# Kernel tuning notes

Hardware: AMD Instinct MI355X
Metric: run time of the kernel (lower is better)

Reference implementation:

```python
import jax, jax.numpy as jnp
import numpy as np

EMBED_DIM = 1024


def setup_inputs() -> dict:
    key = jax.random.key(0)
    ks = jax.random.split(key, 9)
    d = EMBED_DIM
    s = 1.0 / np.sqrt(d)
    x = jax.random.normal(ks[0], (4, 2048, d), dtype=jnp.float32)
    # nn.Linear weights are [out, in]; we store them transposed for x @ W
    Wq = jax.random.uniform(ks[1], (d, d), jnp.float32, -s, s)
    bq = jax.random.uniform(ks[2], (d,), jnp.float32, -s, s)
    Wk = jax.random.uniform(ks[3], (d, d), jnp.float32, -s, s)
    bk = jax.random.uniform(ks[4], (d,), jnp.float32, -s, s)
    Wv = jax.random.uniform(ks[5], (d, d), jnp.float32, -s, s)
    bv = jax.random.uniform(ks[6], (d,), jnp.float32, -s, s)
    Wo = jax.random.uniform(ks[7], (d, d), jnp.float32, -s, s)
    bo = jax.random.uniform(ks[8], (d,), jnp.float32, -s, s)
    return {"x": x, "Wq": Wq, "bq": bq, "Wk": Wk, "bk": bk,
            "Wv": Wv, "bv": bv, "Wo": Wo, "bo": bo}


def reference(x, Wq, bq, Wk, bk, Wv, bv, Wo, bo):
    b, seq_len, d = x.shape
    scaling = 1.0 / jnp.sqrt(jnp.float32(d))
    q = x @ Wq + bq  # [b, s, d]
    k = x @ Wk + bk
    v = x @ Wv + bv
    scores = jnp.einsum('bqd,bkd->bqk', q, k) * scaling  # [b, s, s]
    causal = jnp.tril(jnp.ones((seq_len, seq_len), dtype=bool))
    scores = jnp.where(causal, scores, -jnp.inf)
    attn = jax.nn.softmax(scores, axis=-1)
    out = jnp.einsum('bqk,bkd->bqd', attn, v)
    return out @ Wo + bo
```

## Files before the change

### kernel.cpp

```cpp
#include <hip/hip_runtime.h>
#include <stdint.h>

typedef __bf16 bf16_t;
typedef __bf16 bf16x8 __attribute__((ext_vector_type(8)));
typedef __bf16 bf16x4 __attribute__((ext_vector_type(4)));
typedef float  f32x4  __attribute__((ext_vector_type(4)));

#define DEV __device__ __forceinline__

constexpr int S = 2048, D = 1024, BATCH = 4, MF = BATCH * S;

DEV void gload16(const void* g, void* l) {
  __builtin_amdgcn_global_load_lds(
      (const __attribute__((address_space(1))) void*)g,
      (__attribute__((address_space(3))) void*)(uint32_t)(uintptr_t)l,
      16, 0, 0);
}

template<int EP>
__global__ __launch_bounds__(256, 4) void gemm_core(
    const bf16_t* __restrict__ A, const bf16_t* __restrict__ B,
    void* __restrict__ C0, void* __restrict__ C1, void* __restrict__ C2,
    const float* __restrict__ aux, float* __restrict__ part,
    int M, int N, int K, long sA, long sB)
{
  int tm = blockIdx.x, tn = blockIdx.y;
  const int bz = blockIdx.z;
  if (EP == 2) {
    const int t = blockIdx.x;
    tm = (int)((sqrtf(8.0f * t + 1.0f) - 1.0f) * 0.5f);
    while ((tm + 1) * (tm + 2) / 2 <= t) ++tm;
    while (tm * (tm + 1) / 2 > t) --tm;
    tn = t - tm * (tm + 1) / 2;
  }
  if (EP == 3) tm = (int)gridDim.x - 1 - blockIdx.x;
  const int m0 = tm * 128, n0 = tn * 128;
  int kmax = K;
  if (EP == 3) { int t = m0 + 128; kmax = t < K ? t : K; }
  A += (long)bz * sA;
  B += (long)bz * sB;

  __shared__ __align__(16) bf16_t ldsA[128 * 64];
  __shared__ __align__(16) bf16_t ldsB[128 * 64];

  const int tid  = threadIdx.x;
  const int lane = tid & 63;
  const int wave = tid >> 6;
  const int wm = wave & 1, wn = wave >> 1;
  const int l8r = lane >> 3;
  const int swz = ((lane & 7) ^ (lane >> 3)) * 8;
  const int cl  = lane & 15;
  const int qd  = lane >> 4;
  const int ch0 = ((qd ^ (cl & 7)) * 8);

  f32x4 acc[4][4] = {};

  for (int k0 = 0; k0 < kmax; k0 += 64) {
    #pragma unroll
    for (int t = 0; t < 4; ++t) {
      const int rb = wave * 4 + t;
      gload16(A + (long)(m0 + rb * 8 + l8r) * K + (k0 + swz), &ldsA[rb * 512]);
      gload16(B + (long)(n0 + rb * 8 + l8r) * K + (k0 + swz), &ldsB[rb * 512]);
    }
    __syncthreads();
    #pragma unroll
    for (int kk = 0; kk < 64; kk += 32) {
      bf16x8 af[4], bg[4];
      #pragma unroll
      for (int i = 0; i < 4; ++i)
        af[i] = *(const bf16x8*)&ldsA[(wm * 64 + i * 16 + cl) * 64 + (ch0 ^ kk)];
      #pragma unroll
      for (int j = 0; j < 4; ++j)
        bg[j] = *(const bf16x8*)&ldsB[(wn * 64 + j * 16 + cl) * 64 + (ch0 ^ kk)];
      #pragma unroll
      for (int i = 0; i < 4; ++i)
        #pragma unroll
        for (int j = 0; j < 4; ++j)
          acc[i][j] = __builtin_amdgcn_mfma_f32_16x16x32_bf16(af[i], bg[j], acc[i][j], 0, 0, 0);
    }
    __syncthreads();
  }

  #pragma unroll
  for (int i = 0; i < 4; ++i) {
    const int gm0 = m0 + wm * 64 + i * 16 + qd * 4;

    if (EP == 0) {
      float* Co = (float*)C0;
      #pragma unroll
      for (int j = 0; j < 4; ++j) {
        const int gn = n0 + wn * 64 + j * 16 + cl;
        const float bn = aux[gn];
        #pragma unroll
        for (int r = 0; r < 4; ++r)
          Co[(long)(gm0 + r) * D + gn] = acc[i][j][r] + bn;
      }
    }

    if (EP == 1) {
      bf16_t* q  = (bf16_t*)C0;
      bf16_t* k  = (bf16_t*)C1;
      bf16_t* vT = (bf16_t*)C2;
      #pragma unroll
      for (int j = 0; j < 4; ++j) {
        const int gn  = n0 + wn * 64 + j * 16 + cl;
        const int sec = gn >> 10, ln = gn & 1023;
        const float bn = aux[gn];
        if (sec == 2) {
          const int z = gm0 >> 11, s0 = gm0 & 2047;
          bf16x4 v4;
          #pragma unroll
          for (int r = 0; r < 4; ++r) v4[r] = (bf16_t)(acc[i][j][r] + bn);
          *(bf16x4*)&vT[((long)z * D + ln) * S + s0] = v4;
        } else {
          bf16_t* dst = (sec == 0) ? q : k;
          #pragma unroll
          for (int r = 0; r < 4; ++r)
            dst[(long)(gm0 + r) * D + ln] = (bf16_t)(acc[i][j][r] + bn);
        }
      }
    }

    if (EP == 2) {
      bf16_t* probs = (bf16_t*)C0 + (long)bz * S * S;
      float ls[4] = {0.f, 0.f, 0.f, 0.f};
      #pragma unroll
      for (int j = 0; j < 4; ++j) {
        const int gn = n0 + wn * 64 + j * 16 + cl;
        #pragma unroll
        for (int r = 0; r < 4; ++r) {
          const int gm = gm0 + r;
          const float e = (gn <= gm) ? __expf(acc[i][j][r] * 0.03125f) : 0.0f;
          probs[(long)gm * S + gn] = (bf16_t)e;
          ls[r] += e;
        }
      }
      #pragma unroll
      for (int r = 0; r < 4; ++r) {
        float v = ls[r];
        v += __shfl_xor(v, 1); v += __shfl_xor(v, 2);
        v += __shfl_xor(v, 4); v += __shfl_xor(v, 8);
        if (cl == 0)
          part[((long)bz * S + (gm0 + r)) * 32 + tn * 2 + wn] = v;
      }
    }

    if (EP == 3) {
      bf16_t* attn = (bf16_t*)C0 + (long)bz * S * D;
      const float* invl = aux + (long)bz * S;
      float scl[4];
      #pragma unroll
      for (int r = 0; r < 4; ++r) scl[r] = invl[gm0 + r];
      #pragma unroll
      for (int j = 0; j < 4; ++j) {
        const int gn = n0 + wn * 64 + j * 16 + cl;
        #pragma unroll
        for (int r = 0; r < 4; ++r)
          attn[(long)(gm0 + r) * D + gn] = (bf16_t)(acc[i][j][r] * scl[r]);
      }
    }
  }
}

__global__ __launch_bounds__(256) void reduce_invl(
    const float* __restrict__ part, float* __restrict__ invl)
{
  const int r = blockIdx.x * 256 + threadIdx.x;
  const int row = r & (S - 1);
  const int cnt = ((row >> 7) + 1) * 2;
  const float* p = part + (long)r * 32;
  float s = 0.f;
  for (int j = 0; j < cnt; ++j) s += p[j];
  invl[r] = 1.0f / s;
}

__global__ __launch_bounds__(256) void cvt_x(
    const float4* __restrict__ in, bf16x4* __restrict__ out, int n4)
{
  const int i = blockIdx.x * 256 + threadIdx.x;
  if (i >= n4) return;
  float4 f = in[i];
  bf16x4 o;
  o.x = (__bf16)f.x; o.y = (__bf16)f.y; o.z = (__bf16)f.z; o.w = (__bf16)f.w;
  out[i] = o;
}

__global__ __launch_bounds__(256) void cvt_w_t4(
    const float* __restrict__ W0, const float* __restrict__ W1,
    const float* __restrict__ W2, const float* __restrict__ W3,
    bf16_t* __restrict__ dst)
{
  const float* W = (blockIdx.z == 0) ? W0 : (blockIdx.z == 1) ? W1
                 : (blockIdx.z == 2) ? W2 : W3;
  bf16_t* WT = dst + (size_t)blockIdx.z * D * D;
  __shared__ float t[32][33];
  const int bx = blockIdx.x, by = blockIdx.y;
  const int tx = threadIdx.x & 31, ty = threadIdx.x >> 5;
  #pragma unroll
  for (int dy = 0; dy < 32; dy += 8)
    t[ty + dy][tx] = W[(long)(by * 32 + ty + dy) * 1024 + bx * 32 + tx];
  __syncthreads();
  #pragma unroll
  for (int dy = 0; dy < 32; dy += 8)
    WT[(long)(bx * 32 + ty + dy) * 1024 + by * 32 + tx] = (bf16_t)t[tx][ty + dy];
}

__global__ __launch_bounds__(256) void stack_bias(
    const float* __restrict__ bq, const float* __restrict__ bk,
    const float* __restrict__ bv, float* __restrict__ o)
{
  const int i = blockIdx.x * 256 + threadIdx.x;
  const float* s = (i < 1024) ? bq : (i < 2048) ? bk : bv;
  o[i] = s[i & 1023];
}

extern "C" void kernel_launch(void* const* d_in, const int* in_sizes, int n_in,
                              void* d_out, int out_size, void* d_ws, size_t ws_size,
                              hipStream_t stream) {
  const float* x  = (const float*)d_in[0];
  const float* Wq = (const float*)d_in[1];
  const float* bq = (const float*)d_in[2];
  const float* Wk = (const float*)d_in[3];
  const float* bk = (const float*)d_in[4];
  const float* Wv = (const float*)d_in[5];
  const float* bv = (const float*)d_in[6];
  const float* Wo = (const float*)d_in[7];
  const float* bo = (const float*)d_in[8];
  float* out = (float*)d_out;

  size_t off = 0;
  auto alloc = [&](size_t bytes) -> void* {
    void* p = (char*)d_ws + off;
    off += (bytes + 255) & ~(size_t)255;
    return p;
  };
  bf16_t* x_b   = (bf16_t*)alloc((size_t)MF * D * 2);
  bf16_t* Wall  = (bf16_t*)alloc((size_t)4 * D * D * 2);
  float*  bqkv  = (float*) alloc((size_t)3 * D * 4);
  bf16_t* q_b   = (bf16_t*)alloc((size_t)MF * D * 2);
  bf16_t* k_b   = (bf16_t*)alloc((size_t)MF * D * 2);
  bf16_t* vT_b  = (bf16_t*)alloc((size_t)BATCH * D * S * 2);
  bf16_t* probs = (bf16_t*)alloc((size_t)BATCH * S * S * 2);
  float*  part  = (float*) alloc((size_t)MF * 32 * 4);
  float*  invl  = (float*) alloc((size_t)MF * 4);
  bf16_t* attn  = (bf16_t*)alloc((size_t)MF * D * 2);
  bf16_t* WqkvT = Wall;
  bf16_t* WoT   = Wall + (size_t)3 * D * D;

  cvt_x<<<dim3((MF * D / 4 + 255) / 256), 256, 0, stream>>>(
      (const float4*)x, (bf16x4*)x_b, MF * D / 4);
  cvt_w_t4<<<dim3(32, 32, 4), 256, 0, stream>>>(Wq, Wk, Wv, Wo, Wall);
  stack_bias<<<dim3(12), 256, 0, stream>>>(bq, bk, bv, bqkv);

  gemm_core<1><<<dim3(MF / 128, 3 * D / 128, 1), 256, 0, stream>>>(
      x_b, WqkvT, q_b, k_b, vT_b, bqkv, nullptr, MF, 3 * D, D, 0, 0);

  gemm_core<2><<<dim3(136, 1, BATCH), 256, 0, stream>>>(
      q_b, k_b, probs, nullptr, nullptr, nullptr, part,
      S, S, D, (long)S * D, (long)S * D);

  reduce_invl<<<dim3(MF / 256), 256, 0, stream>>>(part, invl);

  gemm_core<3><<<dim3(S / 128, D / 128, BATCH), 256, 0, stream>>>(
      probs, vT_b, attn, nullptr, nullptr, invl, nullptr,
      S, D, S, (long)S * S, (long)D * S);

  gemm_core<0><<<dim3(MF / 128, D / 128, 1), 256, 0, stream>>>(
      attn, WoT, out, nullptr, nullptr, bo, nullptr, MF, D, D, 0, 0);
}
```

Measured before the change: 280.1 us.

## Split GEMM kernel into per-stage launches with XCD-aware tile scheduling

The templated GEMM is refactored into a shared device body with four dedicated kernels. The QKV projection now runs 768 blocks that each compute two tiles. The score and PV kernels map block ids so that each batch sits on a pair of XCDs (via l&7), which is meant to improve L2 reuse. The PV kernel also interleaves long and short causal rows so that each XCD gets a balanced amount of work. The risk is that the tile mapping leaves some XCDs idle or that the two-tile loop hurts occupancy balance.

```diff
diff --git a/kernel.cpp b/kernel.cpp
--- a/kernel.cpp
+++ b/kernel.cpp
@@ -18,31 +18,14 @@
 }
 
 template<int EP>
-__global__ __launch_bounds__(256, 4) void gemm_core(
-    const bf16_t* __restrict__ A, const bf16_t* __restrict__ B,
-    void* __restrict__ C0, void* __restrict__ C1, void* __restrict__ C2,
-    const float* __restrict__ aux, float* __restrict__ part,
-    int M, int N, int K, long sA, long sB)
-{
-  int tm = blockIdx.x, tn = blockIdx.y;
-  const int bz = blockIdx.z;
-  if (EP == 2) {
-    const int t = blockIdx.x;
-    tm = (int)((sqrtf(8.0f * t + 1.0f) - 1.0f) * 0.5f);
-    while ((tm + 1) * (tm + 2) / 2 <= t) ++tm;
-    while (tm * (tm + 1) / 2 > t) --tm;
-    tn = t - tm * (tm + 1) / 2;
-  }
-  if (EP == 3) tm = (int)gridDim.x - 1 - blockIdx.x;
+DEV void gemm_body(int tm, int tn, int bz,
+                   const bf16_t* __restrict__ A, const bf16_t* __restrict__ B,
+                   void* __restrict__ C0, void* __restrict__ C1,
+                   void* __restrict__ C2, const float* __restrict__ aux,
+                   float* __restrict__ part, int K, int kmax,
+                   bf16_t* ldsA, bf16_t* ldsB)
+{
   const int m0 = tm * 128, n0 = tn * 128;
-  int kmax = K;
-  if (EP == 3) { int t = m0 + 128; kmax = t < K ? t : K; }
-  A += (long)bz * sA;
-  B += (long)bz * sB;
-
-  __shared__ __align__(16) bf16_t ldsA[128 * 64];
-  __shared__ __align__(16) bf16_t ldsB[128 * 64];
-
   const int tid  = threadIdx.x;
   const int lane = tid & 63;
   const int wave = tid >> 6;
@@ -160,6 +143,58 @@
       }
     }
   }
+}
+
+__global__ __launch_bounds__(256, 4) void gemm_qkv(
+    const bf16_t* __restrict__ A, const bf16_t* __restrict__ B,
+    bf16_t* q, bf16_t* k, bf16_t* vT, const float* __restrict__ bias)
+{
+  __shared__ __align__(16) bf16_t lA[128 * 64], lB[128 * 64];
+  #pragma unroll
+  for (int t = 0; t < 2; ++t) {
+    const int l = (int)blockIdx.x + t * 768;
+    gemm_body<1>(l & 63, l >> 6, 0, A, B, q, k, vT, bias, nullptr,
+                 1024, 1024, lA, lB);
+  }
+}
+
+__global__ __launch_bounds__(256, 4) void gemm_sc(
+    const bf16_t* __restrict__ q, const bf16_t* __restrict__ k,
+    bf16_t* probs, float* part)
+{
+  __shared__ __align__(16) bf16_t lA[128 * 64], lB[128 * 64];
+  const int l = blockIdx.x, xcd = l & 7, idx = l >> 3;
+  const int bz = xcd >> 1;
+  const int t  = (xcd & 1) * 68 + idx;
+  int tm = (int)((sqrtf(8.0f * t + 1.0f) - 1.0f) * 0.5f);
+  while ((tm + 1) * (tm + 2) / 2 <= t) ++tm;
+  while (tm * (tm + 1) / 2 > t) --tm;
+  const int tn = t - tm * (tm + 1) / 2;
+  gemm_body<2>(tm, tn, bz, q + (long)bz * S * D, k + (long)bz * S * D,
+               probs, nullptr, nullptr, nullptr, part, 1024, 1024, lA, lB);
+}
+
+__global__ __launch_bounds__(256, 4) void gemm_pv(
+    const bf16_t* __restrict__ probs, const bf16_t* __restrict__ vT,
+    bf16_t* attn, const float* __restrict__ invl)
+{
+  __shared__ __align__(16) bf16_t lA[128 * 64], lB[128 * 64];
+  const int l = blockIdx.x, xcd = l & 7, idx = l >> 3;
+  const int bz = xcd >> 1, half = xcd & 1;
+  const int slot = idx >> 3, tn = idx & 7;
+  const int tm = (slot & 1) ? (slot - 1 + half) : (15 - half - slot);
+  const int kmax = (tm + 1) * 128;
+  gemm_body<3>(tm, tn, bz, probs + (long)bz * S * S, vT + (long)bz * D * S,
+               attn, nullptr, nullptr, invl, nullptr, 2048, kmax, lA, lB);
+}
+
+__global__ __launch_bounds__(256, 4) void gemm_oproj(
+    const bf16_t* __restrict__ attn, const bf16_t* __restrict__ WoT,
+    float* out, const float* __restrict__ bo)
+{
+  __shared__ __align__(16) bf16_t lA[128 * 64], lB[128 * 64];
+  gemm_body<0>(blockIdx.x, blockIdx.y, 0, attn, WoT, out, nullptr, nullptr,
+               bo, nullptr, 1024, 1024, lA, lB);
 }
 
 __global__ __launch_bounds__(256) void reduce_invl(
@@ -252,19 +287,13 @@
   cvt_w_t4<<<dim3(32, 32, 4), 256, 0, stream>>>(Wq, Wk, Wv, Wo, Wall);
   stack_bias<<<dim3(12), 256, 0, stream>>>(bq, bk, bv, bqkv);
 
-  gemm_core<1><<<dim3(MF / 128, 3 * D / 128, 1), 256, 0, stream>>>(
-      x_b, WqkvT, q_b, k_b, vT_b, bqkv, nullptr, MF, 3 * D, D, 0, 0);
-
-  gemm_core<2><<<dim3(136, 1, BATCH), 256, 0, stream>>>(
-      q_b, k_b, probs, nullptr, nullptr, nullptr, part,
-      S, S, D, (long)S * D, (long)S * D);
+  gemm_qkv<<<dim3(768), 256, 0, stream>>>(x_b, WqkvT, q_b, k_b, vT_b, bqkv);
+
+  gemm_sc<<<dim3(544), 256, 0, stream>>>(q_b, k_b, probs, part);
 
   reduce_invl<<<dim3(MF / 256), 256, 0, stream>>>(part, invl);
 
-  gemm_core<3><<<dim3(S / 128, D / 128, BATCH), 256, 0, stream>>>(
-      probs, vT_b, attn, nullptr, nullptr, invl, nullptr,
-      S, D, S, (long)S * S, (long)D * S);
-
-  gemm_core<0><<<dim3(MF / 128, D / 128, 1), 256, 0, stream>>>(
-      attn, WoT, out, nullptr, nullptr, bo, nullptr, MF, D, D, 0, 0);
-}
+  gemm_pv<<<dim3(512), 256, 0, stream>>>(probs, vT_b, attn, invl);
+
+  gemm_oproj<<<dim3(64, 8), 256, 0, stream>>>(attn, WoT, out, bo);
+}
```

Result: faster. 251.7 us (-10.2%).
